# Kernel optimization log

Hardware: AMD Instinct MI355X
Metric: run time of the kernel (lower is better)

Reference implementation:

```python
import jax, jax.numpy as jnp
import numpy as np

D_MODEL = 1024
D_STATE = 16
D_CONV = 4
EXPAND = 2
D_INNER = EXPAND * D_MODEL  # 2048
DT_RANK = 16  # per source: list(range(1,17))[-1] since d_inner >= 16
BATCH = 2
SEQ = 1024


def setup_inputs() -> dict:
    key = jax.random.key(0)
    ks = jax.random.split(key, 8)
    s = 0.02
    return {
        "x": jax.random.normal(ks[0], (BATCH, SEQ, D_MODEL), jnp.float32),
        # torch Linear convention: weight [out, in]
        "in_proj_w": jax.random.normal(ks[1], (2 * D_INNER, D_MODEL), jnp.float32) * s,
        "in_proj_b": jnp.zeros((2 * D_INNER,), jnp.float32),
        # depthwise conv: [d_inner, 1, d_conv]
        "conv_w": jax.random.normal(ks[2], (D_INNER, 1, D_CONV), jnp.float32) * s,
        "conv_b": jnp.zeros((D_INNER,), jnp.float32),
        "x_proj_w": jax.random.normal(ks[3], (DT_RANK + 2 * D_STATE, D_INNER), jnp.float32) * s,
        "x_proj_b": jnp.zeros((DT_RANK + 2 * D_STATE,), jnp.float32),
        "dt_proj_w": jax.random.normal(ks[4], (D_INNER, DT_RANK), jnp.float32) * s,
        "dt_proj_b": jnp.zeros((D_INNER,), jnp.float32),
        "A_log": jnp.log(jnp.broadcast_to(jnp.arange(1, D_STATE + 1, dtype=jnp.float32), (D_INNER, D_STATE))),
        "D": jnp.ones((D_INNER,), jnp.float32),
        "out_proj_w": jax.random.normal(ks[5], (D_MODEL, D_INNER), jnp.float32) * s,
        "out_proj_b": jnp.zeros((D_MODEL,), jnp.float32),
    }


def _mamba(x, in_proj_w, in_proj_b, conv_w, conv_b, x_proj_w, x_proj_b,
           dt_proj_w, dt_proj_b, A_log, D, out_proj_w, out_proj_b):
    # in_proj and split into x / res branches
    x_and_res = x @ in_proj_w.T + in_proj_b                       # [B, L, 2*d_inner]
    xs, res = jnp.split(x_and_res, [D_INNER], axis=-1)
    # causal depthwise conv: left-pad d_conv-1, which matches padding=d_conv-1 then [:, :, :l]
    xc = jnp.transpose(xs, (0, 2, 1))                             # [B, d_inner, L]
    xc = jax.lax.conv_general_dilated(
        xc, conv_w, window_strides=(1,), padding=[(D_CONV - 1, 0)],
        feature_group_count=D_INNER, dimension_numbers=("NCH", "OIH", "NCH"))
    xc = xc + conv_b[None, :, None]
    xs = jax.nn.silu(jnp.transpose(xc, (0, 2, 1)))                # [B, L, d_inner]

    # SSM input-dependent parameters
    x_dbl = xs @ x_proj_w.T + x_proj_b                            # [B, L, dt_rank + 2n]
    dlt, Bm, Cm = jnp.split(x_dbl, [DT_RANK, DT_RANK + D_STATE], axis=-1)
    delta = jax.nn.softplus(dlt @ dt_proj_w.T + dt_proj_b)        # [B, L, d_inner]
    A = -jnp.exp(A_log)                                           # [d_inner, n]

    # selective scan over time
    def step(h, inputs):
        d_t, x_t, b_t, c_t = inputs                               # [B,d],[B,d],[B,n],[B,n]
        dA = jnp.exp(d_t[:, :, None] * A)                         # [B, d, n]
        h = dA * h + (d_t * x_t)[:, :, None] * b_t[:, None, :]    # [B, d, n]
        y_t = jnp.einsum("bdn,bn->bd", h, c_t)                   # [B, d]
        return h, y_t

    h0 = jnp.zeros((xs.shape[0], D_INNER, D_STATE), xs.dtype)
    seq_inputs = (jnp.moveaxis(delta, 1, 0), jnp.moveaxis(xs, 1, 0),
                  jnp.moveaxis(Bm, 1, 0), jnp.moveaxis(Cm, 1, 0))
    _, ys = jax.lax.scan(step, h0, seq_inputs)                    # ys: [L, B, d_inner]
    y = jnp.moveaxis(ys, 0, 1) + xs * D                           # skip term D

    y = y * jax.nn.silu(res)                                      # gating
    return y @ out_proj_w.T + out_proj_b                          # [B, L, d_model]


def reference(x, in_proj_w, in_proj_b, conv_w, conv_b, x_proj_w, x_proj_b,
              dt_proj_w, dt_proj_b, A_log, D, out_proj_w, out_proj_b):
    return _mamba(x, in_proj_w, in_proj_b, conv_w, conv_b, x_proj_w, x_proj_b,
                  dt_proj_w, dt_proj_b, A_log, D, out_proj_w, out_proj_b)
```

## Files before the change

kernel.cpp:

```cpp
#include <hip/hip_runtime.h>

#define D_MODEL 1024
#define D_STATE 16
#define D_CONV  4
#define D_INNER 2048
#define DT_RANK 16
#define BATCH   2
#define SEQ     1024
#define M_ROWS  (BATCH*SEQ)
#define CHUNK   32
#define NCHUNK  (SEQ/CHUNK)
#define XP_KSPLIT 16
#define XP_KLEN (D_INNER / XP_KSPLIT)

typedef __bf16 bf16x8 __attribute__((ext_vector_type(8)));
typedef float  f32x4  __attribute__((ext_vector_type(4)));

__device__ __forceinline__ unsigned short f2bf(float f) {
  unsigned u = __float_as_uint(f);
  u += 0x7fffu + ((u >> 16) & 1u);
  return (unsigned short)(u >> 16);
}

__device__ __forceinline__ float sigmoid_fast(float v) {
  return 1.f / (1.f + __expf(-v));
}

__device__ __forceinline__ float softplus_f(float s) {
  return (s > 20.f) ? s : __logf(1.f + __expf(s));
}

__device__ __forceinline__ void gll16(const void* g, void* l) {
  __builtin_amdgcn_global_load_lds(
      (const __attribute__((address_space(1))) unsigned int*)g,
      (__attribute__((address_space(3))) unsigned int*)l, 16, 0, 0);
}

__device__ __forceinline__ void storeC(float v, float* p)          { *p = v; }
__device__ __forceinline__ void storeC(float v, unsigned short* p) { *p = f2bf(v); }

__global__ __launch_bounds__(256) void cast_all_kernel(
    const float* __restrict__ x, const float* __restrict__ w1, const float* __restrict__ w2,
    const float* __restrict__ xpw,
    unsigned short* __restrict__ xbf, unsigned short* __restrict__ w1bf,
    unsigned short* __restrict__ w2bf, unsigned short* __restrict__ xpwbf,
    float* __restrict__ zbuf ) {
  const int N0 = (M_ROWS * D_MODEL) / 4;
  const int N1 = (2 * D_INNER * D_MODEL) / 4;
  const int N2 = (D_MODEL * D_INNER) / 4;
  const int N3 = (48 * D_INNER) / 4;
  int i = blockIdx.x * 256 + threadIdx.x;
  const float* src; unsigned short* dst; int off;
  if (i < N0)                 { src = x;   dst = xbf;   off = i; }
  else if (i < N0 + N1)       { src = w1;  dst = w1bf;  off = i - N0; }
  else if (i < N0 + N1 + N2)  { src = w2;  dst = w2bf;  off = i - N0 - N1; }
  else if (i < N0 + N1 + N2 + N3) { src = xpw; dst = xpwbf; off = i - N0 - N1 - N2; }
  else {
    float4 z = {0.f, 0.f, 0.f, 0.f};
    ((float4*)zbuf)[i - N0 - N1 - N2 - N3] = z;
    return;
  }
  float4 v = *(const float4*)(src + (size_t)off * 4);
  ushort4 o;
  o.x = f2bf(v.x); o.y = f2bf(v.y); o.z = f2bf(v.z); o.w = f2bf(v.w);
  *(ushort4*)(dst + (size_t)off * 4) = o;
}

template<int BM, int BK, typename CT>
__global__ __launch_bounds__(256) void gemm_gll(
    const __bf16* __restrict__ A, const __bf16* __restrict__ B,
    const float* __restrict__ bias, CT* __restrict__ C,
    int M, int N, int K) {
  constexpr int MR  = BM / 32;
  constexpr int LPR = BK / 8;
  constexpr int RPI = 64 / LPR;
  __shared__ __bf16 As[BM][BK];
  __shared__ __bf16 Bs[128][BK];
  const int tid  = threadIdx.x;
  const int lane = tid & 63;
  const int w    = tid >> 6;
  const int wr   = w >> 1, wc = w & 1;
  const int rowBase = blockIdx.y * BM;
  const int colBase = blockIdx.x * 128;

  f32x4 acc[MR][4];
  #pragma unroll
  for (int i = 0; i < MR; ++i)
    #pragma unroll
    for (int j = 0; j < 4; ++j) { f32x4 z = {0.f,0.f,0.f,0.f}; acc[i][j] = z; }

  const int srow = lane / LPR;
  const int sk   = (lane % LPR) * 8;
  const int fr   = lane & 15;
  const int fk   = (lane >> 4) * 8;

  for (int k0 = 0; k0 < K; k0 += BK) {
    #pragma unroll
    for (int i = 0; i < BM / RPI / 4; ++i) {
      const int r0 = w * (BM / 4) + i * RPI;
      gll16(A + (size_t)(rowBase + r0 + srow) * K + k0 + sk, &As[r0][0]);
    }
    #pragma unroll
    for (int i = 0; i < 128 / RPI / 4; ++i) {
      const int r0 = w * 32 + i * RPI;
      gll16(B + (size_t)(colBase + r0 + srow) * K + k0 + sk, &Bs[r0][0]);
    }
    __syncthreads();

    #pragma unroll
    for (int kk = 0; kk < BK / 32; ++kk) {
      bf16x8 af[MR], bfr[4];
      #pragma unroll
      for (int mm = 0; mm < MR; ++mm)
        af[mm] = *(const bf16x8*)&As[wr * (BM / 2) + mm * 16 + fr][kk * 32 + fk];
      #pragma unroll
      for (int nn = 0; nn < 4; ++nn)
        bfr[nn] = *(const bf16x8*)&Bs[wc * 64 + nn * 16 + fr][kk * 32 + fk];
      #pragma unroll
      for (int mm = 0; mm < MR; ++mm)
        #pragma unroll
        for (int nn = 0; nn < 4; ++nn)
          acc[mm][nn] = __builtin_amdgcn_mfma_f32_16x16x32_bf16(af[mm], bfr[nn], acc[mm][nn], 0, 0, 0);
    }
    __syncthreads();
  }

  #pragma unroll
  for (int nn = 0; nn < 4; ++nn) {
    int col = colBase + wc * 64 + nn * 16 + fr;
    float bv = bias[col];
    #pragma unroll
    for (int mm = 0; mm < MR; ++mm) {
      int row0 = rowBase + wr * (BM / 2) + mm * 16 + (lane >> 4) * 4;
      #pragma unroll
      for (int r = 0; r < 4; ++r)
        storeC(acc[mm][nn][r] + bv, &C[(size_t)(row0 + r) * N + col]);
    }
  }
}

__global__ __launch_bounds__(256) void conv_silu_kernel(
    const unsigned short* __restrict__ xar, const float* __restrict__ cw,
    const float* __restrict__ cb, unsigned short* __restrict__ xsbf) {
  int idx = blockIdx.x * 256 + threadIdx.x;
  int m  = idx >> 8;
  int d8 = (idx & 255) << 3;
  int t  = m & (SEQ - 1);
  const __bf16* xarb = (const __bf16*)xar;

  float4 cwl[8];
  const float4* cw4 = (const float4*)cw;
  #pragma unroll
  for (int e = 0; e < 8; ++e) cwl[e] = cw4[d8 + e];

  float acc[8];
  #pragma unroll
  for (int e = 0; e < 8; ++e) acc[e] = cb[d8 + e];

  #pragma unroll
  for (int j = 0; j < 4; ++j) {
    int tt = t - 3 + j;
    if (tt < 0) continue;
    bf16x8 v = *(const bf16x8*)&xarb[(size_t)(m - 3 + j) * (2 * D_INNER) + d8];
    const float* cj = (const float*)cwl;
    #pragma unroll
    for (int e = 0; e < 8; ++e)
      acc[e] += (float)v[e] * cj[e * 4 + j];
  }
  unsigned short o[8];
  #pragma unroll
  for (int e = 0; e < 8; ++e) {
    float s = acc[e] * sigmoid_fast(acc[e]);
    o[e] = f2bf(s);
  }
  *(ushort4*)&xsbf[(size_t)m * D_INNER + d8]     = *(ushort4*)&o[0];
  *(ushort4*)&xsbf[(size_t)m * D_INNER + d8 + 4] = *(ushort4*)&o[4];
}

__global__ __launch_bounds__(256) void xproj_mfma(
    const __bf16* __restrict__ A, const __bf16* __restrict__ B,
    const float* __restrict__ xpb,
    float* __restrict__ dlt, float* __restrict__ Bm, float* __restrict__ Cm) {
  __shared__ __bf16 As[64][32];
  __shared__ __bf16 Bs[48][32];
  const int tid  = threadIdx.x;
  const int lane = tid & 63;
  const int w    = tid >> 6;
  const int rowBase = blockIdx.x * 64;
  const int kbase   = blockIdx.y * XP_KLEN;

  f32x4 acc[3];
  #pragma unroll
  for (int j = 0; j < 3; ++j) { f32x4 z = {0.f,0.f,0.f,0.f}; acc[j] = z; }

  const int srow = lane >> 2;
  const int sk   = (lane & 3) * 8;
  const int fr   = lane & 15;
  const int fk   = (lane >> 4) * 8;

  for (int k0 = kbase; k0 < kbase + XP_KLEN; k0 += 32) {
    gll16(A + (size_t)(rowBase + w * 16 + srow) * D_INNER + k0 + sk, &As[w * 16][0]);
    if (w < 3)
      gll16(B + (size_t)(w * 16 + srow) * D_INNER + k0 + sk, &Bs[w * 16][0]);
    __syncthreads();
    bf16x8 af = *(const bf16x8*)&As[w * 16 + fr][fk];
    #pragma unroll
    for (int nn = 0; nn < 3; ++nn) {
      bf16x8 bv = *(const bf16x8*)&Bs[nn * 16 + fr][fk];
      acc[nn] = __builtin_amdgcn_mfma_f32_16x16x32_bf16(af, bv, acc[nn], 0, 0, 0);
    }
    __syncthreads();
  }

  const int c16 = lane & 15;
  const float biasOn = (blockIdx.y == 0) ? 1.f : 0.f;
  #pragma unroll
  for (int nn = 0; nn < 3; ++nn) {
    float bv = biasOn * xpb[nn * 16 + c16];
    float* dst = (nn == 0) ? dlt : (nn == 1) ? Bm : Cm;
    int row0 = rowBase + w * 16 + (lane >> 4) * 4;
    #pragma unroll
    for (int r = 0; r < 4; ++r)
      atomicAdd(&dst[(size_t)(row0 + r) * 16 + c16], acc[nn][r] + bv);
  }
}


#define DELTA16(sarr, ttq)                                                       \
  {                                                                              \
    float4 q0 = *(const float4*)&sarr[ttq][0];                                   \
    float4 q1 = *(const float4*)&sarr[ttq][4];                                   \
    float4 q2 = *(const float4*)&sarr[ttq][8];                                   \
    float4 q3 = *(const float4*)&sarr[ttq][12];                                  \
    s += q0.x*dtwr[0] + q0.y*dtwr[1] + q0.z*dtwr[2] + q0.w*dtwr[3];              \
    s += q1.x*dtwr[4] + q1.y*dtwr[5] + q1.z*dtwr[6] + q1.w*dtwr[7];              \
    s += q2.x*dtwr[8] + q2.y*dtwr[9] + q2.z*dtwr[10] + q2.w*dtwr[11];            \
    s += q3.x*dtwr[12] + q3.y*dtwr[13] + q3.z*dtwr[14] + q3.w*dtwr[15];          \
  }

__global__ __launch_bounds__(256) void scan_phase1(
    const unsigned short* __restrict__ xsbf, const float* __restrict__ dlt,
    const float* __restrict__ Bmat, const float* __restrict__ dtw,
    const float* __restrict__ dtb, const float* __restrict__ alog,
    float* __restrict__ Hbuf, float* __restrict__ Sbuf) {
  __shared__ float dltS[CHUNK][16];
  __shared__ float BS[CHUNK][16];
  const int tid = threadIdx.x;
  const int c   = blockIdx.y;
  const int b   = blockIdx.z;
  const int d   = blockIdx.x * 256 + tid;
  const int row0 = b * SEQ + c * CHUNK;
  const __bf16* xsb16 = (const __bf16*)xsbf;
  {
    int e = tid * 2;
    int tt = e >> 4, r = e & 15;
    *(float2*)&dltS[tt][r] = *(const float2*)&dlt[(row0 + tt) * 16 + r];
    *(float2*)&BS[tt][r]   = *(const float2*)&Bmat[(row0 + tt) * 16 + r];
  }
  float dtwr[16], An[16];
  #pragma unroll
  for (int q = 0; q < 4; ++q) {
    float4 w4 = *(const float4*)&dtw[d * 16 + q * 4];
    dtwr[q*4+0] = w4.x; dtwr[q*4+1] = w4.y; dtwr[q*4+2] = w4.z; dtwr[q*4+3] = w4.w;
    float4 a4 = *(const float4*)&alog[d * 16 + q * 4];
    An[q*4+0] = -__expf(a4.x); An[q*4+1] = -__expf(a4.y);
    An[q*4+2] = -__expf(a4.z); An[q*4+3] = -__expf(a4.w);
  }
  const float dtbv = dtb[d];
  float xv[CHUNK];
  #pragma unroll
  for (int tt = 0; tt < CHUNK; ++tt)
    xv[tt] = (float)xsb16[(size_t)(row0 + tt) * D_INNER + d];
  __syncthreads();
  float dv[CHUNK];
  #pragma unroll
  for (int tt = 0; tt < CHUNK; ++tt) {
    float s = dtbv;
    DELTA16(dltS, tt);
    dv[tt] = softplus_f(s);
  }
  float h[16];
  #pragma unroll
  for (int n = 0; n < 16; ++n) h[n] = 0.f;
  float Ssum = 0.f;
  #pragma unroll
  for (int tt = 0; tt < CHUNK; ++tt) {
    const float dvt = dv[tt];
    Ssum += dvt;
    const float dvx = dvt * xv[tt];
    float4 B0 = *(const float4*)&BS[tt][0];
    float4 B1 = *(const float4*)&BS[tt][4];
    float4 B2 = *(const float4*)&BS[tt][8];
    float4 B3 = *(const float4*)&BS[tt][12];
    h[0]  = __expf(dvt*An[0])*h[0]   + dvx*B0.x;
    h[1]  = __expf(dvt*An[1])*h[1]   + dvx*B0.y;
    h[2]  = __expf(dvt*An[2])*h[2]   + dvx*B0.z;
    h[3]  = __expf(dvt*An[3])*h[3]   + dvx*B0.w;
    h[4]  = __expf(dvt*An[4])*h[4]   + dvx*B1.x;
    h[5]  = __expf(dvt*An[5])*h[5]   + dvx*B1.y;
    h[6]  = __expf(dvt*An[6])*h[6]   + dvx*B1.z;
    h[7]  = __expf(dvt*An[7])*h[7]   + dvx*B1.w;
    h[8]  = __expf(dvt*An[8])*h[8]   + dvx*B2.x;
    h[9]  = __expf(dvt*An[9])*h[9]   + dvx*B2.y;
    h[10] = __expf(dvt*An[10])*h[10] + dvx*B2.z;
    h[11] = __expf(dvt*An[11])*h[11] + dvx*B2.w;
    h[12] = __expf(dvt*An[12])*h[12] + dvx*B3.x;
    h[13] = __expf(dvt*An[13])*h[13] + dvx*B3.y;
    h[14] = __expf(dvt*An[14])*h[14] + dvx*B3.z;
    h[15] = __expf(dvt*An[15])*h[15] + dvx*B3.w;
  }
  size_t hbase = (((size_t)(b * NCHUNK + c) * D_INNER) + d) * 16;
  #pragma unroll
  for (int q = 0; q < 4; ++q) {
    float4 o = {h[q*4+0], h[q*4+1], h[q*4+2], h[q*4+3]};
    *(float4*)&Hbuf[hbase + q*4] = o;
  }
  Sbuf[((size_t)b * NCHUNK + c) * D_INNER + d] = Ssum;
}

__global__ __launch_bounds__(256) void scan_phase2(
    const float* __restrict__ alog, const float* __restrict__ Sbuf,
    float* __restrict__ Hbuf) {
  const int tid = threadIdx.x;
  const int n  = tid & 15;
  const int dl = tid >> 4;
  const int d  = blockIdx.x * 16 + dl;
  const int b  = blockIdx.y;
  const float An = -__expf(alog[d * 16 + n]);
  float h_run = 0.f;
  #pragma unroll 4
  for (int c = 0; c < NCHUNK; ++c) {
    size_t idx = (((size_t)(b * NCHUNK + c) * D_INNER) + d) * 16 + n;
    float hend = Hbuf[idx];
    float P = __expf(An * Sbuf[((size_t)b * NCHUNK + c) * D_INNER + d]);
    Hbuf[idx] = h_run;
    h_run = P * h_run + hend;
  }
}

__global__ __launch_bounds__(256) void scan_phase3(
    const unsigned short* __restrict__ xsbf, const unsigned short* __restrict__ xar,
    const float* __restrict__ dlt, const float* __restrict__ Bmat,
    const float* __restrict__ Cmat, const float* __restrict__ dtw,
    const float* __restrict__ dtb, const float* __restrict__ alog,
    const float* __restrict__ Dvec, const float* __restrict__ Hbuf,
    unsigned short* __restrict__ ybf) {
  __shared__ float dltS[CHUNK][16];
  __shared__ float BS[CHUNK][16];
  __shared__ float CS[CHUNK][16];
  const int tid = threadIdx.x;
  const int c   = blockIdx.y;
  const int b   = blockIdx.z;
  const int d   = blockIdx.x * 256 + tid;
  const int row0 = b * SEQ + c * CHUNK;
  const __bf16* xsb16 = (const __bf16*)xsbf;
  const __bf16* xarb  = (const __bf16*)xar;
  {
    int e = tid * 2;
    int tt = e >> 4, r = e & 15;
    *(float2*)&dltS[tt][r] = *(const float2*)&dlt[(row0 + tt) * 16 + r];
    *(float2*)&BS[tt][r]   = *(const float2*)&Bmat[(row0 + tt) * 16 + r];
    *(float2*)&CS[tt][r]   = *(const float2*)&Cmat[(row0 + tt) * 16 + r];
  }
  float dtwr[16], An[16];
  #pragma unroll
  for (int q = 0; q < 4; ++q) {
    float4 w4 = *(const float4*)&dtw[d * 16 + q * 4];
    dtwr[q*4+0] = w4.x; dtwr[q*4+1] = w4.y; dtwr[q*4+2] = w4.z; dtwr[q*4+3] = w4.w;
    float4 a4 = *(const float4*)&alog[d * 16 + q * 4];
    An[q*4+0] = -__expf(a4.x); An[q*4+1] = -__expf(a4.y);
    An[q*4+2] = -__expf(a4.z); An[q*4+3] = -__expf(a4.w);
  }
  const float dtbv = dtb[d];
  const float Dn   = Dvec[d];
  float h[16];
  {
    size_t hbase = (((size_t)(b * NCHUNK + c) * D_INNER) + d) * 16;
    #pragma unroll
    for (int q = 0; q < 4; ++q) {
      float4 hv = *(const float4*)&Hbuf[hbase + q*4];
      h[q*4+0] = hv.x; h[q*4+1] = hv.y; h[q*4+2] = hv.z; h[q*4+3] = hv.w;
    }
  }
  float xv[CHUNK], rv[CHUNK];
  #pragma unroll
  for (int tt = 0; tt < CHUNK; ++tt) {
    xv[tt] = (float)xsb16[(size_t)(row0 + tt) * D_INNER + d];
    rv[tt] = (float)xarb[(size_t)(row0 + tt) * (2 * D_INNER) + D_INNER + d];
  }
  __syncthreads();
  float dv[CHUNK];
  #pragma unroll
  for (int tt = 0; tt < CHUNK; ++tt) {
    float s = dtbv;
    DELTA16(dltS, tt);
    dv[tt] = softplus_f(s);
  }
  #pragma unroll
  for (int tt = 0; tt < CHUNK; ++tt) {
    const float dvt = dv[tt];
    const float dvx = dvt * xv[tt];
    float4 B0 = *(const float4*)&BS[tt][0];
    float4 B1 = *(const float4*)&BS[tt][4];
    float4 B2 = *(const float4*)&BS[tt][8];
    float4 B3 = *(const float4*)&BS[tt][12];
    float4 C0 = *(const float4*)&CS[tt][0];
    float4 C1 = *(const float4*)&CS[tt][4];
    float4 C2 = *(const float4*)&CS[tt][8];
    float4 C3 = *(const float4*)&CS[tt][12];
    float y = 0.f;
    h[0]  = __expf(dvt*An[0])*h[0]   + dvx*B0.x;  y += h[0]*C0.x;
    h[1]  = __expf(dvt*An[1])*h[1]   + dvx*B0.y;  y += h[1]*C0.y;
    h[2]  = __expf(dvt*An[2])*h[2]   + dvx*B0.z;  y += h[2]*C0.z;
    h[3]  = __expf(dvt*An[3])*h[3]   + dvx*B0.w;  y += h[3]*C0.w;
    h[4]  = __expf(dvt*An[4])*h[4]   + dvx*B1.x;  y += h[4]*C1.x;
    h[5]  = __expf(dvt*An[5])*h[5]   + dvx*B1.y;  y += h[5]*C1.y;
    h[6]  = __expf(dvt*An[6])*h[6]   + dvx*B1.z;  y += h[6]*C1.z;
    h[7]  = __expf(dvt*An[7])*h[7]   + dvx*B1.w;  y += h[7]*C1.w;
    h[8]  = __expf(dvt*An[8])*h[8]   + dvx*B2.x;  y += h[8]*C2.x;
    h[9]  = __expf(dvt*An[9])*h[9]   + dvx*B2.y;  y += h[9]*C2.y;
    h[10] = __expf(dvt*An[10])*h[10] + dvx*B2.z;  y += h[10]*C2.z;
    h[11] = __expf(dvt*An[11])*h[11] + dvx*B2.w;  y += h[11]*C2.w;
    h[12] = __expf(dvt*An[12])*h[12] + dvx*B3.x;  y += h[12]*C3.x;
    h[13] = __expf(dvt*An[13])*h[13] + dvx*B3.y;  y += h[13]*C3.y;
    h[14] = __expf(dvt*An[14])*h[14] + dvx*B3.z;  y += h[14]*C3.z;
    h[15] = __expf(dvt*An[15])*h[15] + dvx*B3.w;  y += h[15]*C3.w;
    y += xv[tt] * Dn;
    const float r = rv[tt];
    const float v = y * (r * sigmoid_fast(r));
    ybf[(size_t)(row0 + tt) * D_INNER + d] = f2bf(v);
  }
}

extern "C" void kernel_launch(void* const* d_in, const int* in_sizes, int n_in,
                              void* d_out, int out_size, void* d_ws, size_t ws_size,
                              hipStream_t stream) {
  const float* x    = (const float*)d_in[0];
  const float* ipw  = (const float*)d_in[1];
  const float* ipb  = (const float*)d_in[2];
  const float* cw   = (const float*)d_in[3];
  const float* cb   = (const float*)d_in[4];
  const float* xpw  = (const float*)d_in[5];
  const float* xpb  = (const float*)d_in[6];
  const float* dtw  = (const float*)d_in[7];
  const float* dtb  = (const float*)d_in[8];
  const float* alog = (const float*)d_in[9];
  const float* Dv   = (const float*)d_in[10];
  const float* opw  = (const float*)d_in[11];
  const float* opb  = (const float*)d_in[12];
  float* out = (float*)d_out;

  char* ws = (char*)d_ws;
  size_t off = 0;
  auto alloc = [&](size_t bytes) {
    char* p = ws + off;
    off += (bytes + 255) & ~(size_t)255;
    return p;
  };
  unsigned short* xbf   = (unsigned short*)alloc((size_t)M_ROWS * D_MODEL * 2);
  unsigned short* w1bf  = (unsigned short*)alloc((size_t)2 * D_INNER * D_MODEL * 2);
  unsigned short* w2bf  = (unsigned short*)alloc((size_t)D_MODEL * D_INNER * 2);
  unsigned short* xpwbf = (unsigned short*)alloc((size_t)48 * D_INNER * 2);
  unsigned short* xar   = (unsigned short*)alloc((size_t)M_ROWS * 2 * D_INNER * 2);
  unsigned short* xsbf  = (unsigned short*)alloc((size_t)M_ROWS * D_INNER * 2);
  float* dlt = (float*)alloc((size_t)M_ROWS * 16 * 4);
  float* Bm  = (float*)alloc((size_t)M_ROWS * 16 * 4);
  float* Cm  = (float*)alloc((size_t)M_ROWS * 16 * 4);
  unsigned short* ybf = (unsigned short*)alloc((size_t)M_ROWS * D_INNER * 2);
  if (off > ws_size) return;
  float* Hbuf = (float*)w1bf;
  float* Sbuf = (float*)xbf;

  cast_all_kernel<<<8384, 256, 0, stream>>>(x, ipw, opw, xpw, xbf, w1bf, w2bf, xpwbf, dlt);
  gemm_gll<128, 64, unsigned short><<<dim3(4096 / 128, 2048 / 128), 256, 0, stream>>>(
      (const __bf16*)xbf, (const __bf16*)w1bf, ipb, xar, M_ROWS, 2 * D_INNER, D_MODEL);
  conv_silu_kernel<<<2048, 256, 0, stream>>>(xar, cw, cb, xsbf);
  xproj_mfma<<<dim3(M_ROWS / 64, XP_KSPLIT), 256, 0, stream>>>(
      (const __bf16*)xsbf, (const __bf16*)xpwbf, xpb, dlt, Bm, Cm);
  scan_phase1<<<dim3(D_INNER / 256, NCHUNK, BATCH), 256, 0, stream>>>(
      xsbf, dlt, Bm, dtw, dtb, alog, Hbuf, Sbuf);
  scan_phase2<<<dim3(D_INNER / 16, BATCH), 256, 0, stream>>>(alog, Sbuf, Hbuf);
  scan_phase3<<<dim3(D_INNER / 256, NCHUNK, BATCH), 256, 0, stream>>>(
      xsbf, xar, dlt, Bm, Cm, dtw, dtb, alog, Dv, Hbuf, ybf);
  gemm_gll<64, 64, float><<<dim3(1024 / 128, 2048 / 64), 256, 0, stream>>>(
      (const __bf16*)ybf, (const __bf16*)w2bf, opb, out, M_ROWS, D_MODEL, D_INNER);
}
```

Before: 249.6 us.

## Fuse conv+SiLU into x_proj kernel and fold scan phase2 into phase1 tail

Computes the causal depthwise conv and SiLU inside the x_proj MFMA kernel, writing the activations directly to LDS for the projection while still storing them globally. It also removes the separate phase2 scan kernel: the last phase1 block per (batch, d-slice), detected via an atomic counter, runs the cross-chunk prefix. This removes one global reread of the activations and two kernel launches. The trade-off is that the chunk-prefix work runs on only 16 blocks, serially over chunks.

```diff
diff --git a/kernel.cpp b/kernel.cpp
--- a/kernel.cpp
+++ b/kernel.cpp
@@ -49,6 +49,7 @@
   const int N1 = (2 * D_INNER * D_MODEL) / 4;
   const int N2 = (D_MODEL * D_INNER) / 4;
   const int N3 = (48 * D_INNER) / 4;
+  const int NZ = (3 * M_ROWS * 16 * 4 + 256) / 16;
   int i = blockIdx.x * 256 + threadIdx.x;
   const float* src; unsigned short* dst; int off;
   if (i < N0)                 { src = x;   dst = xbf;   off = i; }
@@ -56,8 +57,8 @@
   else if (i < N0 + N1 + N2)  { src = w2;  dst = w2bf;  off = i - N0 - N1; }
   else if (i < N0 + N1 + N2 + N3) { src = xpw; dst = xpwbf; off = i - N0 - N1 - N2; }
   else {
-    float4 z = {0.f, 0.f, 0.f, 0.f};
-    ((float4*)zbuf)[i - N0 - N1 - N2 - N3] = z;
+    int zi = i - N0 - N1 - N2 - N3;
+    if (zi < NZ) { float4 z = {0.f,0.f,0.f,0.f}; ((float4*)zbuf)[zi] = z; }
     return;
   }
   float4 v = *(const float4*)(src + (size_t)off * 4);
@@ -139,89 +140,95 @@
   }
 }
 
-__global__ __launch_bounds__(256) void conv_silu_kernel(
+__global__ __launch_bounds__(256) void convxproj_kernel(
     const unsigned short* __restrict__ xar, const float* __restrict__ cw,
-    const float* __restrict__ cb, unsigned short* __restrict__ xsbf) {
-  int idx = blockIdx.x * 256 + threadIdx.x;
-  int m  = idx >> 8;
-  int d8 = (idx & 255) << 3;
-  int t  = m & (SEQ - 1);
-  const __bf16* xarb = (const __bf16*)xar;
-
-  float4 cwl[8];
-  const float4* cw4 = (const float4*)cw;
-  #pragma unroll
-  for (int e = 0; e < 8; ++e) cwl[e] = cw4[d8 + e];
-
-  float acc[8];
-  #pragma unroll
-  for (int e = 0; e < 8; ++e) acc[e] = cb[d8 + e];
-
-  #pragma unroll
-  for (int j = 0; j < 4; ++j) {
-    int tt = t - 3 + j;
-    if (tt < 0) continue;
-    bf16x8 v = *(const bf16x8*)&xarb[(size_t)(m - 3 + j) * (2 * D_INNER) + d8];
-    const float* cj = (const float*)cwl;
-    #pragma unroll
-    for (int e = 0; e < 8; ++e)
-      acc[e] += (float)v[e] * cj[e * 4 + j];
-  }
-  unsigned short o[8];
-  #pragma unroll
-  for (int e = 0; e < 8; ++e) {
-    float s = acc[e] * sigmoid_fast(acc[e]);
-    o[e] = f2bf(s);
-  }
-  *(ushort4*)&xsbf[(size_t)m * D_INNER + d8]     = *(ushort4*)&o[0];
-  *(ushort4*)&xsbf[(size_t)m * D_INNER + d8 + 4] = *(ushort4*)&o[4];
-}
-
-__global__ __launch_bounds__(256) void xproj_mfma(
-    const __bf16* __restrict__ A, const __bf16* __restrict__ B,
-    const float* __restrict__ xpb,
+    const float* __restrict__ cb, const __bf16* __restrict__ B,
+    const float* __restrict__ xpb, unsigned short* __restrict__ xsbf,
     float* __restrict__ dlt, float* __restrict__ Bm, float* __restrict__ Cm) {
-  __shared__ __bf16 As[64][32];
-  __shared__ __bf16 Bs[48][32];
+  __shared__ __bf16 As[64][128];
+  __shared__ __bf16 Bs[48][128];
   const int tid  = threadIdx.x;
   const int lane = tid & 63;
   const int w    = tid >> 6;
-  const int rowBase = blockIdx.x * 64;
-  const int kbase   = blockIdx.y * XP_KLEN;
-
-  f32x4 acc[3];
-  #pragma unroll
-  for (int j = 0; j < 3; ++j) { f32x4 z = {0.f,0.f,0.f,0.f}; acc[j] = z; }
-
-  const int srow = lane >> 2;
-  const int sk   = (lane & 3) * 8;
-  const int fr   = lane & 15;
-  const int fk   = (lane >> 4) * 8;
-
-  for (int k0 = kbase; k0 < kbase + XP_KLEN; k0 += 32) {
-    gll16(A + (size_t)(rowBase + w * 16 + srow) * D_INNER + k0 + sk, &As[w * 16][0]);
-    if (w < 3)
-      gll16(B + (size_t)(w * 16 + srow) * D_INNER + k0 + sk, &Bs[w * 16][0]);
-    __syncthreads();
-    bf16x8 af = *(const bf16x8*)&As[w * 16 + fr][fk];
+  const int r0   = blockIdx.x * 64;
+  const int k0   = blockIdx.y * XP_KLEN;
+  const __bf16* xarb = (const __bf16*)xar;
+
+  {
+    const int srow = lane >> 4;
+    const int sk   = (lane & 15) * 8;
+    #pragma unroll
+    for (int i = 0; i < 3; ++i) {
+      const int rb = w * 12 + i * 4;
+      gll16(B + (size_t)(rb + srow) * D_INNER + k0 + sk, &Bs[rb][0]);
+    }
+  }
+
+  const int dc = (tid & 15) * 8;
+  const int d  = k0 + dc;
+  float4 cwl[8];
+  const float4* cw4 = (const float4*)cw;
+  #pragma unroll
+  for (int e = 0; e < 8; ++e) cwl[e] = cw4[d + e];
+  float cbl[8];
+  #pragma unroll
+  for (int e = 0; e < 8; ++e) cbl[e] = cb[d + e];
+
+  #pragma unroll
+  for (int p = 0; p < 4; ++p) {
+    int ch  = tid + p * 256;
+    int row = ch >> 4;
+    int m   = r0 + row;
+    int t   = m & (SEQ - 1);
+    float acc[8];
+    #pragma unroll
+    for (int e = 0; e < 8; ++e) acc[e] = cbl[e];
+    #pragma unroll
+    for (int j = 0; j < 4; ++j) {
+      int tt = t - 3 + j;
+      if (tt < 0) continue;
+      bf16x8 v = *(const bf16x8*)&xarb[(size_t)(m - 3 + j) * (2 * D_INNER) + d];
+      const float* cj = (const float*)cwl;
+      #pragma unroll
+      for (int e = 0; e < 8; ++e)
+        acc[e] += (float)v[e] * cj[e * 4 + j];
+    }
+    unsigned short o[8];
+    #pragma unroll
+    for (int e = 0; e < 8; ++e) {
+      float s = acc[e] * sigmoid_fast(acc[e]);
+      o[e] = f2bf(s);
+    }
+    *(bf16x8*)&As[row][dc] = *(bf16x8*)&o[0];
+    *(ushort4*)&xsbf[(size_t)m * D_INNER + d]     = *(ushort4*)&o[0];
+    *(ushort4*)&xsbf[(size_t)m * D_INNER + d + 4] = *(ushort4*)&o[4];
+  }
+  __syncthreads();
+
+  f32x4 acc3[3];
+  #pragma unroll
+  for (int j = 0; j < 3; ++j) { f32x4 z = {0.f,0.f,0.f,0.f}; acc3[j] = z; }
+  const int fr = lane & 15;
+  const int fk = (lane >> 4) * 8;
+  #pragma unroll
+  for (int kk = 0; kk < 4; ++kk) {
+    bf16x8 af = *(const bf16x8*)&As[w * 16 + fr][kk * 32 + fk];
     #pragma unroll
     for (int nn = 0; nn < 3; ++nn) {
-      bf16x8 bv = *(const bf16x8*)&Bs[nn * 16 + fr][fk];
-      acc[nn] = __builtin_amdgcn_mfma_f32_16x16x32_bf16(af, bv, acc[nn], 0, 0, 0);
-    }
-    __syncthreads();
-  }
-
-  const int c16 = lane & 15;
+      bf16x8 bv = *(const bf16x8*)&Bs[nn * 16 + fr][kk * 32 + fk];
+      acc3[nn] = __builtin_amdgcn_mfma_f32_16x16x32_bf16(af, bv, acc3[nn], 0, 0, 0);
+    }
+  }
+
   const float biasOn = (blockIdx.y == 0) ? 1.f : 0.f;
   #pragma unroll
   for (int nn = 0; nn < 3; ++nn) {
-    float bv = biasOn * xpb[nn * 16 + c16];
+    float bv = biasOn * xpb[nn * 16 + fr];
     float* dst = (nn == 0) ? dlt : (nn == 1) ? Bm : Cm;
-    int row0 = rowBase + w * 16 + (lane >> 4) * 4;
+    int row0 = r0 + w * 16 + (lane >> 4) * 4;
     #pragma unroll
     for (int r = 0; r < 4; ++r)
-      atomicAdd(&dst[(size_t)(row0 + r) * 16 + c16], acc[nn][r] + bv);
+      atomicAdd(&dst[(size_t)(row0 + r) * 16 + fr], acc3[nn][r] + bv);
   }
 }
 
@@ -242,9 +249,10 @@
     const unsigned short* __restrict__ xsbf, const float* __restrict__ dlt,
     const float* __restrict__ Bmat, const float* __restrict__ dtw,
     const float* __restrict__ dtb, const float* __restrict__ alog,
-    float* __restrict__ Hbuf, float* __restrict__ Sbuf) {
+    float* __restrict__ Hbuf, float* __restrict__ Sbuf, int* __restrict__ cnt) {
   __shared__ float dltS[CHUNK][16];
   __shared__ float BS[CHUNK][16];
+  __shared__ int lastFlag;
   const int tid = threadIdx.x;
   const int c   = blockIdx.y;
   const int b   = blockIdx.z;
@@ -316,25 +324,34 @@
     *(float4*)&Hbuf[hbase + q*4] = o;
   }
   Sbuf[((size_t)b * NCHUNK + c) * D_INNER + d] = Ssum;
-}
-
-__global__ __launch_bounds__(256) void scan_phase2(
-    const float* __restrict__ alog, const float* __restrict__ Sbuf,
-    float* __restrict__ Hbuf) {
-  const int tid = threadIdx.x;
-  const int n  = tid & 15;
-  const int dl = tid >> 4;
-  const int d  = blockIdx.x * 16 + dl;
-  const int b  = blockIdx.y;
-  const float An = -__expf(alog[d * 16 + n]);
-  float h_run = 0.f;
-  #pragma unroll 4
-  for (int c = 0; c < NCHUNK; ++c) {
-    size_t idx = (((size_t)(b * NCHUNK + c) * D_INNER) + d) * 16 + n;
-    float hend = Hbuf[idx];
-    float P = __expf(An * Sbuf[((size_t)b * NCHUNK + c) * D_INNER + d]);
-    Hbuf[idx] = h_run;
-    h_run = P * h_run + hend;
+
+  __threadfence();
+  __syncthreads();
+  if (tid == 0)
+    lastFlag = (atomicAdd(&cnt[b * 8 + blockIdx.x], 1) == NCHUNK - 1) ? 1 : 0;
+  __syncthreads();
+  if (!lastFlag) return;
+  __threadfence();
+
+  const int n2  = tid & 15;
+  const int dl2 = tid >> 4;
+  float hr[16], An2[16];
+  #pragma unroll
+  for (int q = 0; q < 16; ++q) {
+    int dq = blockIdx.x * 256 + dl2 + q * 16;
+    An2[q] = -__expf(alog[dq * 16 + n2]);
+    hr[q] = 0.f;
+  }
+  for (int c2 = 0; c2 < NCHUNK; ++c2) {
+    #pragma unroll
+    for (int q = 0; q < 16; ++q) {
+      int dq = blockIdx.x * 256 + dl2 + q * 16;
+      size_t idx = (((size_t)(b * NCHUNK + c2) * D_INNER) + dq) * 16 + n2;
+      float hend = Hbuf[idx];
+      float P = __expf(An2[q] * Sbuf[((size_t)b * NCHUNK + c2) * D_INNER + dq]);
+      Hbuf[idx] = hr[q];
+      hr[q] = P * hr[q] + hend;
+    }
   }
 }
 
@@ -466,20 +483,19 @@
   float* dlt = (float*)alloc((size_t)M_ROWS * 16 * 4);
   float* Bm  = (float*)alloc((size_t)M_ROWS * 16 * 4);
   float* Cm  = (float*)alloc((size_t)M_ROWS * 16 * 4);
+  int*   cnt = (int*)alloc(256);
   unsigned short* ybf = (unsigned short*)alloc((size_t)M_ROWS * D_INNER * 2);
   if (off > ws_size) return;
   float* Hbuf = (float*)w1bf;
   float* Sbuf = (float*)xbf;
 
-  cast_all_kernel<<<8384, 256, 0, stream>>>(x, ipw, opw, xpw, xbf, w1bf, w2bf, xpwbf, dlt);
+  cast_all_kernel<<<8385, 256, 0, stream>>>(x, ipw, opw, xpw, xbf, w1bf, w2bf, xpwbf, dlt);
   gemm_gll<128, 64, unsigned short><<<dim3(4096 / 128, 2048 / 128), 256, 0, stream>>>(
       (const __bf16*)xbf, (const __bf16*)w1bf, ipb, xar, M_ROWS, 2 * D_INNER, D_MODEL);
-  conv_silu_kernel<<<2048, 256, 0, stream>>>(xar, cw, cb, xsbf);
-  xproj_mfma<<<dim3(M_ROWS / 64, XP_KSPLIT), 256, 0, stream>>>(
-      (const __bf16*)xsbf, (const __bf16*)xpwbf, xpb, dlt, Bm, Cm);
+  convxproj_kernel<<<dim3(M_ROWS / 64, XP_KSPLIT), 256, 0, stream>>>(
+      xar, cw, cb, (const __bf16*)xpwbf, xpb, xsbf, dlt, Bm, Cm);
   scan_phase1<<<dim3(D_INNER / 256, NCHUNK, BATCH), 256, 0, stream>>>(
-      xsbf, dlt, Bm, dtw, dtb, alog, Hbuf, Sbuf);
-  scan_phase2<<<dim3(D_INNER / 16, BATCH), 256, 0, stream>>>(alog, Sbuf, Hbuf);
+      xsbf, dlt, Bm, dtw, dtb, alog, Hbuf, Sbuf, cnt);
   scan_phase3<<<dim3(D_INNER / 256, NCHUNK, BATCH), 256, 0, stream>>>(
       xsbf, xar, dlt, Bm, Cm, dtw, dtb, alog, Dv, Hbuf, ybf);
   gemm_gll<64, 64, float><<<dim3(1024 / 128, 2048 / 64), 256, 0, stream>>>(
```

Result: slower. 325.7 us (+30.5%).
